# Kernel tuning notes

Measured on AMD Instinct MI355X. Metric: run time of the kernel, lower is better.

Reference implementation:

```python
import jax, jax.numpy as jnp
import numpy as np


def setup_inputs() -> dict:
    key = jax.random.key(0)
    k1, k2, k3, k4 = jax.random.split(key, 4)
    B, T_dec, T_enc, H2 = 8, 64, 512, 512  # H2 = 2*hiddenSize
    encoderOutput = jax.random.normal(k1, (B, T_enc, H2), dtype=jnp.float32)
    decoderInput = jax.random.normal(k2, (B, T_dec, H2), dtype=jnp.float32)
    # fc: Linear(4H -> 2H); torch weight layout [out, in] = [2H, 4H]
    W = jax.random.normal(k3, (H2, 2 * H2), dtype=jnp.float32) * (1.0 / np.sqrt(2 * H2))
    b = jax.random.normal(k4, (H2,), dtype=jnp.float32) * 0.01
    return {"encoderOutput": encoderOutput, "decoderInput": decoderInput, "W": W, "b": b}


def reference(encoderOutput, decoderInput, W, b):
    # Original: for each (i, j), fc(cat(dec[:,i], enc[:,j])) then log_softmax over
    # the FEATURE dim (dim=1 of the flattened [-1, 2H] tensor), then
    # context[:, i] = sum_j log_softmax(...) * enc[:, j].
    H2 = encoderOutput.shape[-1]
    W_dec = W[:, :H2]   # columns multiplying the decoder half of the concat
    W_enc = W[:, H2:]   # columns multiplying the encoder half
    dec_part = jnp.einsum('bid,od->bio', decoderInput, W_dec)   # [B, T_dec, 2H]
    enc_part = jnp.einsum('bjd,od->bjo', encoderOutput, W_enc)  # [B, T_enc, 2H]
    logits = dec_part[:, :, None, :] + enc_part[:, None, :, :] + b  # [B, T_dec, T_enc, 2H]
    alpha = jax.nn.log_softmax(logits, axis=-1)  # softmax over feature dim, as in source
    context = jnp.einsum('bijd,bjd->bid', alpha, encoderOutput)  # [B, T_dec, 2H]
    return context
```

## Files before the change

kernel.cpp:

```cpp
#include <hip/hip_runtime.h>


namespace {
constexpr int kH  = 512;
constexpr int kTD = 64;
constexpr int kTE = 512;
constexpr int kB  = 8;
constexpr int kRD = kB * kTD;
constexpr int kRE = kB * kTE;
}

typedef __attribute__((ext_vector_type(8))) short short8;
typedef __attribute__((ext_vector_type(4))) float floatx4;

__device__ __forceinline__ unsigned short f2bf(float x) {
    unsigned u = __float_as_uint(x);
    u += 0x7fffu + ((u >> 16) & 1u);
    return (unsigned short)(u >> 16);
}
__device__ __forceinline__ float bf2f(unsigned short h) {
    return __uint_as_float(((unsigned)h) << 16);
}

__global__ __launch_bounds__(256) void fused_cast(
    const float* __restrict__ W, const float* __restrict__ dec,
    const float* __restrict__ enc,
    unsigned short* __restrict__ Wd, unsigned short* __restrict__ We,
    unsigned short* __restrict__ dec_bf,
    unsigned short* __restrict__ enc_bf, unsigned short* __restrict__ encT,
    float* __restrict__ S1, float* __restrict__ S2)
{
    const int blk = blockIdx.x, t = threadIdx.x;
    if (blk < 2048) {
        const int idx = blk * 256 + t;
        const int row = idx >> 10, col = idx & 1023;
        const unsigned short v = f2bf(W[idx]);
        if (col < kH) Wd[row * kH + col] = v;
        else          We[row * kH + (col - kH)] = v;
        if (idx < kRD * kH) dec_bf[idx] = f2bf(dec[idx]);
        if (idx < kB * kH) { S1[idx] = 0.f; S2[idx] = 0.f; }
    } else {
        __shared__ unsigned short s[32][33];
        const int tid = blk - 2048;
        const int b = tid >> 8, rem = tid & 255;
        const int j0 = (rem >> 4) * 32, d0 = (rem & 15) * 32;
        const int tx = t & 31, ty = t >> 5;
        const float* src = enc + ((size_t)b * kTE + j0) * kH + d0;
        unsigned short* edst = enc_bf + ((size_t)b * kTE + j0) * kH + d0;
#pragma unroll
        for (int jj = 0; jj < 32; jj += 8) {
            const unsigned short h = f2bf(src[(size_t)(ty + jj) * kH + tx]);
            s[ty + jj][tx] = h;
            edst[(size_t)(ty + jj) * kH + tx] = h;
        }
        __syncthreads();
        unsigned short* tdst = encT + ((size_t)b * kH + d0) * kTE + j0;
#pragma unroll
        for (int dd = 0; dd < 32; dd += 8)
            tdst[(size_t)(ty + dd) * kTE + tx] = s[tx][ty + dd];
    }
}

__global__ __launch_bounds__(256) void gemm1(
    const unsigned short* __restrict__ enc_bf,
    const unsigned short* __restrict__ dec_bf,
    const unsigned short* __restrict__ Wd,
    const unsigned short* __restrict__ We,
    const float* __restrict__ bias,
    unsigned short* __restrict__ part_bf, unsigned short* __restrict__ uv)
{
    const int tile = blockIdx.x;
    const int ns = tile & 7, ms = tile >> 3;
    const int t = threadIdx.x, w = t >> 6, l = t & 63;
    const int qm = w >> 1, qn = w & 1;
    const int lr = l & 15, lq = l >> 4;
    const bool isenc = (ms >= 8);
    const unsigned short* A = isenc ? (enc_bf + (size_t)(ms - 8) * 64 * kH)
                                    : (dec_bf + (size_t)ms * 64 * kH);
    const unsigned short* Bw = isenc ? We : Wd;
    const unsigned short* a0 = A + (size_t)(qm * 32 + lr) * kH + lq * 8;
    const unsigned short* b0 = Bw + (size_t)(ns * 64 + qn * 32 + lr) * kH + lq * 8;

    floatx4 acc[2][2];
#pragma unroll
    for (int m = 0; m < 2; ++m)
#pragma unroll
        for (int n = 0; n < 2; ++n) acc[m][n] = (floatx4){0.f, 0.f, 0.f, 0.f};

    for (int k0 = 0; k0 < kH; k0 += 32) {
        short8 af[2], bf[2];
#pragma unroll
        for (int m = 0; m < 2; ++m) af[m] = *(const short8*)(a0 + (size_t)m * 16 * kH + k0);
#pragma unroll
        for (int n = 0; n < 2; ++n) bf[n] = *(const short8*)(b0 + (size_t)n * 16 * kH + k0);
#pragma unroll
        for (int m = 0; m < 2; ++m)
#pragma unroll
            for (int n = 0; n < 2; ++n)
                acc[m][n] = __builtin_amdgcn_mfma_f32_16x16x32_bf16(af[m], bf[n], acc[m][n], 0, 0, 0);
    }

    const int rowbase = ms * 64 + qm * 32, colbase = ns * 64 + qn * 32;
#pragma unroll
    for (int n = 0; n < 2; ++n) {
        const int col = colbase + n * 16 + lr;
        const float bv = isenc ? bias[col] : 0.f;
#pragma unroll
        for (int m = 0; m < 2; ++m) {
            const int row0 = rowbase + m * 16 + lq * 4;
#pragma unroll
            for (int r = 0; r < 4; ++r) {
                const float v = acc[m][n][r];
                const size_t off = (size_t)(row0 + r) * kH + col;
                part_bf[off] = f2bf(v);
                uv[off]      = f2bf(__expf(v + bv));
            }
        }
    }
}

__global__ __launch_bounds__(256) void lse_s1s2(
    const unsigned short* __restrict__ uv, unsigned short* __restrict__ lse_bf,
    const float* __restrict__ enc, const unsigned short* __restrict__ part_bf,
    float* __restrict__ S1, float* __restrict__ S2)
{
    __shared__ float red[4][16][68];
    const int blk = blockIdx.x, t = threadIdx.x;
    if (blk < 256) {
        const int b = blk >> 5, rem = blk & 31;
        const int it = rem >> 3, jt = rem & 7;
        const int w = t >> 6, l = t & 63;
        const int lr = l & 15, lq = l >> 4;
        const unsigned short* ua = uv + (size_t)(b * 64 + it * 16 + lr) * kH + w * 128 + lq * 8;
        const unsigned short* vb = uv + (size_t)(kRD + b * kTE + jt * 64 + lr) * kH + w * 128 + lq * 8;

        floatx4 acc[4];
#pragma unroll
        for (int n = 0; n < 4; ++n) acc[n] = (floatx4){0.f, 0.f, 0.f, 0.f};
#pragma unroll
        for (int k0 = 0; k0 < 128; k0 += 32) {
            const short8 af = *(const short8*)(ua + k0);
#pragma unroll
            for (int n = 0; n < 4; ++n)
                acc[n] = __builtin_amdgcn_mfma_f32_16x16x32_bf16(
                    af, *(const short8*)(vb + (size_t)n * 16 * kH + k0), acc[n], 0, 0, 0);
        }
#pragma unroll
        for (int n = 0; n < 4; ++n)
#pragma unroll
            for (int r = 0; r < 4; ++r)
                red[w][lq * 4 + r][n * 16 + lr] = acc[n][r];
        __syncthreads();
        const int i = t >> 4, j0 = (t & 15) * 4;
        float4 s = *(const float4*)&red[0][i][j0];
        const float4 s1 = *(const float4*)&red[1][i][j0];
        const float4 s2 = *(const float4*)&red[2][i][j0];
        const float4 s3 = *(const float4*)&red[3][i][j0];
        s.x += s1.x + s2.x + s3.x; s.y += s1.y + s2.y + s3.y;
        s.z += s1.z + s2.z + s3.z; s.w += s1.w + s2.w + s3.w;
        ushort4 o;
        o.x = f2bf(__logf(s.x)); o.y = f2bf(__logf(s.y));
        o.z = f2bf(__logf(s.z)); o.w = f2bf(__logf(s.w));
        *(ushort4*)(lse_bf + (size_t)(b * kTD + it * 16 + i) * kTE + jt * 64 + j0) = o;
    } else {
        const int blk2 = blk - 256;
        const int jc = blk2 & 15, b = (blk2 >> 4) & 7, dh = blk2 >> 7;
        const int d = dh * 256 + t;
        const float* e = enc + ((size_t)b * kTE + jc * 32) * kH + d;
        const unsigned short* p = part_bf + (size_t)(kRD + b * kTE + jc * 32) * kH + d;
        float s1 = 0.f, s2 = 0.f;
#pragma unroll 4
        for (int j = 0; j < 32; ++j) {
            const float ev = e[(size_t)j * kH];
            const float pv = bf2f(p[(size_t)j * kH]);
            s1 += ev;
            s2 = fmaf(pv, ev, s2);
        }
        atomicAdd(&S1[b * kH + d], s1);
        atomicAdd(&S2[b * kH + d], s2);
    }
}

__global__ __launch_bounds__(256) void final_k(
    const unsigned short* __restrict__ lse_bf,
    const unsigned short* __restrict__ encT,
    const unsigned short* __restrict__ part_bf,
    const float* __restrict__ bias,
    const float* __restrict__ S1, const float* __restrict__ S2,
    float* __restrict__ out)
{
    __shared__ float red[4][16][68];
    const int blk = blockIdx.x, t = threadIdx.x;
    const int b = blk >> 5, rem = blk & 31;
    const int it = rem >> 3, dt = rem & 7;
    const int w = t >> 6, l = t & 63;
    const int lr = l & 15, lq = l >> 4;
    const unsigned short* la = lse_bf + (size_t)(b * kTD + it * 16 + lr) * kTE + w * 128 + lq * 8;
    const unsigned short* eb = encT + ((size_t)b * kH + dt * 64 + lr) * kTE + w * 128 + lq * 8;

    floatx4 acc[4];
#pragma unroll
    for (int n = 0; n < 4; ++n) acc[n] = (floatx4){0.f, 0.f, 0.f, 0.f};
#pragma unroll
    for (int k0 = 0; k0 < 128; k0 += 32) {
        const short8 af = *(const short8*)(la + k0);
#pragma unroll
        for (int n = 0; n < 4; ++n)
            acc[n] = __builtin_amdgcn_mfma_f32_16x16x32_bf16(
                af, *(const short8*)(eb + (size_t)n * 16 * kTE + k0), acc[n], 0, 0, 0);
    }
#pragma unroll
    for (int n = 0; n < 4; ++n)
#pragma unroll
        for (int r = 0; r < 4; ++r)
            red[w][lq * 4 + r][n * 16 + lr] = acc[n][r];
    __syncthreads();
    const int i = t >> 4, d0 = (t & 15) * 4;
    float4 m = *(const float4*)&red[0][i][d0];
    const float4 m1 = *(const float4*)&red[1][i][d0];
    const float4 m2 = *(const float4*)&red[2][i][d0];
    const float4 m3 = *(const float4*)&red[3][i][d0];
    m.x += m1.x + m2.x + m3.x; m.y += m1.y + m2.y + m3.y;
    m.z += m1.z + m2.z + m3.z; m.w += m1.w + m2.w + m3.w;

    const int gd = dt * 64 + d0;
    const float4 s1 = *(const float4*)(S1 + b * kH + gd);
    const float4 s2 = *(const float4*)(S2 + b * kH + gd);
    const float4 bi = *(const float4*)(bias + gd);
    const int row = b * kTD + it * 16 + i;
    const ushort4 dp = *(const ushort4*)(part_bf + (size_t)row * kH + gd);
    float4 o;
    o.x = fmaf(bf2f(dp.x) + bi.x, s1.x, s2.x) - m.x;
    o.y = fmaf(bf2f(dp.y) + bi.y, s1.y, s2.y) - m.y;
    o.z = fmaf(bf2f(dp.z) + bi.z, s1.z, s2.z) - m.z;
    o.w = fmaf(bf2f(dp.w) + bi.w, s1.w, s2.w) - m.w;
    *(float4*)(out + (size_t)row * kH + gd) = o;
}

extern "C" void kernel_launch(void* const* d_in, const int* in_sizes, int n_in,
                              void* d_out, int out_size, void* d_ws, size_t ws_size,
                              hipStream_t stream)
{
    (void)in_sizes; (void)n_in; (void)out_size; (void)ws_size;
    const float* enc  = (const float*)d_in[0];
    const float* dec  = (const float*)d_in[1];
    const float* W    = (const float*)d_in[2];
    const float* bias = (const float*)d_in[3];
    float* out = (float*)d_out;

    char* base = (char*)d_ws;
    unsigned short* part_bf = (unsigned short*)(base);
    unsigned short* uv      = (unsigned short*)(base + 4718592);
    unsigned short* enc_bf  = (unsigned short*)(base + 9437184);
    unsigned short* encT    = (unsigned short*)(base + 13631488);
    unsigned short* dec_bf  = (unsigned short*)(base + 17825792);
    unsigned short* Wd      = (unsigned short*)(base + 18350080);
    unsigned short* We      = (unsigned short*)(base + 18874368);
    unsigned short* lse_bf  = (unsigned short*)(base + 19398656);
    float*          S1      = (float*)(base + 19922944);
    float*          S2      = (float*)(base + 19939328);

    fused_cast<<<4096, 256, 0, stream>>>(W, dec, enc, Wd, We, dec_bf,
                                         enc_bf, encT, S1, S2);
    gemm1<<<576, 256, 0, stream>>>(enc_bf, dec_bf, Wd, We, bias, part_bf, uv);
    lse_s1s2<<<512, 256, 0, stream>>>(uv, lse_bf, enc, part_bf, S1, S2);
    final_k<<<256, 256, 0, stream>>>(lse_bf, encT, part_bf, bias, S1, S2, out);
}
```

Before: 102.7 us.

## Store bf16 operands in MFMA fragment-tiled layout across all kernels

Every bf16 intermediate (W halves, decoder, encoder, transposed encoder, exp-logits, lse) is now written in a fragment-packed layout, so each lane loads one contiguous 16-byte fragment and each wave reads one contiguous 1 KB block instead of strided rows. The cast kernel is rewritten to do vectorized float4 loads with packed short8 stores, which cuts its grid from 4096 to 1408 blocks. The gemm1 epilogue is staged through shared memory so its stores are vectorized. This adds an LDS round trip and more complex indexing, and the layouts of the producer and consumer kernels must agree exactly.

```diff
diff --git a/kernel.cpp b/kernel.cpp
--- a/kernel.cpp
+++ b/kernel.cpp
@@ -21,108 +21,161 @@
 __device__ __forceinline__ float bf2f(unsigned short h) {
     return __uint_as_float(((unsigned)h) << 16);
 }
+__device__ __forceinline__ size_t fragTile(int rtile, int kt) {
+    return ((size_t)rtile * 16 + kt) * 512;
+}
+__device__ __forceinline__ short8 pack8(float4 a, float4 b) {
+    short8 r;
+    r[0] = (short)f2bf(a.x); r[1] = (short)f2bf(a.y);
+    r[2] = (short)f2bf(a.z); r[3] = (short)f2bf(a.w);
+    r[4] = (short)f2bf(b.x); r[5] = (short)f2bf(b.y);
+    r[6] = (short)f2bf(b.z); r[7] = (short)f2bf(b.w);
+    return r;
+}
 
 __global__ __launch_bounds__(256) void fused_cast(
     const float* __restrict__ W, const float* __restrict__ dec,
     const float* __restrict__ enc,
-    unsigned short* __restrict__ Wd, unsigned short* __restrict__ We,
-    unsigned short* __restrict__ dec_bf,
-    unsigned short* __restrict__ enc_bf, unsigned short* __restrict__ encT,
-    float* __restrict__ S1, float* __restrict__ S2)
+    unsigned short* __restrict__ Wd_f, unsigned short* __restrict__ We_f,
+    unsigned short* __restrict__ dec_f,
+    unsigned short* __restrict__ enc_f, unsigned short* __restrict__ encT_f,
+    float* __restrict__ S12)
 {
     const int blk = blockIdx.x, t = threadIdx.x;
-    if (blk < 2048) {
-        const int idx = blk * 256 + t;
-        const int row = idx >> 10, col = idx & 1023;
-        const unsigned short v = f2bf(W[idx]);
-        if (col < kH) Wd[row * kH + col] = v;
-        else          We[row * kH + (col - kH)] = v;
-        if (idx < kRD * kH) dec_bf[idx] = f2bf(dec[idx]);
-        if (idx < kB * kH) { S1[idx] = 0.f; S2[idx] = 0.f; }
+    const int w = t >> 6, l = t & 63;
+    const int lr = l & 15, lc = l >> 4;
+    if (blk < 256) {
+        const int gw = blk * 4 + w;
+        const int sel = gw >> 9, rem = gw & 511;
+        const int ot = rem >> 4, kt = rem & 15;
+        const int o = ot * 16 + lr;
+        const float* src = W + (size_t)o * 1024 + sel * 512 + kt * 32 + lc * 8;
+        const float4 v0 = *(const float4*)src;
+        const float4 v1 = *(const float4*)(src + 4);
+        unsigned short* dst = (sel ? We_f : Wd_f) + fragTile(ot, kt) + l * 8;
+        *(short8*)dst = pack8(v0, v1);
+        if (blk < 32) S12[blk * 256 + t] = 0.f;
+    } else if (blk < 384) {
+        const int gw = (blk - 256) * 4 + w;
+        const int rt = gw >> 4, kt = gw & 15;
+        const int r = rt * 16 + lr;
+        const float* src = dec + (size_t)r * kH + kt * 32 + lc * 8;
+        const float4 v0 = *(const float4*)src;
+        const float4 v1 = *(const float4*)(src + 4);
+        *(short8*)(dec_f + fragTile(rt, kt) + l * 8) = pack8(v0, v1);
     } else {
-        __shared__ unsigned short s[32][33];
-        const int tid = blk - 2048;
-        const int b = tid >> 8, rem = tid & 255;
-        const int j0 = (rem >> 4) * 32, d0 = (rem & 15) * 32;
-        const int tx = t & 31, ty = t >> 5;
-        const float* src = enc + ((size_t)b * kTE + j0) * kH + d0;
-        unsigned short* edst = enc_bf + ((size_t)b * kTE + j0) * kH + d0;
-#pragma unroll
-        for (int jj = 0; jj < 32; jj += 8) {
-            const unsigned short h = f2bf(src[(size_t)(ty + jj) * kH + tx]);
-            s[ty + jj][tx] = h;
-            edst[(size_t)(ty + jj) * kH + tx] = h;
-        }
+        __shared__ unsigned short s[64][36];
+        const int e = blk - 384;
+        const int kt = e & 15, jt = (e >> 4) & 7, b = e >> 7;
+        const int j0 = jt * 64, d0 = kt * 32;
+        const int jl = w * 16 + lr;
+        const float* src = enc + ((size_t)(b * kTE + j0 + jl)) * kH + d0 + lc * 8;
+        const float4 v0 = *(const float4*)src;
+        const float4 v1 = *(const float4*)(src + 4);
+        const short8 p = pack8(v0, v1);
+        *(short8*)(enc_f + fragTile(b * 32 + jt * 4 + w, kt) + l * 8) = p;
+#pragma unroll
+        for (int i = 0; i < 8; ++i) s[jl][lc * 8 + i] = (unsigned short)p[i];
         __syncthreads();
-        unsigned short* tdst = encT + ((size_t)b * kH + d0) * kTE + j0;
-#pragma unroll
-        for (int dd = 0; dd < 32; dd += 8)
-            tdst[(size_t)(ty + dd) * kTE + tx] = s[tx][ty + dd];
+        const int dt = w >> 1, jc = w & 1;
+        const int dl = dt * 16 + lr;
+        const int j8 = jc * 32 + lc * 8;
+        short8 v;
+#pragma unroll
+        for (int i = 0; i < 8; ++i) v[i] = (short)s[j8 + i][dl];
+        *(short8*)(encT_f + fragTile(b * 32 + kt * 2 + dt, jt * 2 + jc) + l * 8) = v;
     }
 }
 
 __global__ __launch_bounds__(256) void gemm1(
-    const unsigned short* __restrict__ enc_bf,
-    const unsigned short* __restrict__ dec_bf,
-    const unsigned short* __restrict__ Wd,
-    const unsigned short* __restrict__ We,
+    const unsigned short* __restrict__ enc_f,
+    const unsigned short* __restrict__ dec_f,
+    const unsigned short* __restrict__ Wd_f,
+    const unsigned short* __restrict__ We_f,
     const float* __restrict__ bias,
-    unsigned short* __restrict__ part_bf, unsigned short* __restrict__ uv)
-{
+    unsigned short* __restrict__ part_bf, unsigned short* __restrict__ uv_f)
+{
+    __shared__ float As[64][68];
     const int tile = blockIdx.x;
     const int ns = tile & 7, ms = tile >> 3;
     const int t = threadIdx.x, w = t >> 6, l = t & 63;
     const int qm = w >> 1, qn = w & 1;
+    const bool isenc = (ms >= 8);
+    const unsigned short* A = isenc ? enc_f : dec_f;
+    const unsigned short* Bw = isenc ? We_f : Wd_f;
+    const int art = (isenc ? (ms - 8) : ms) * 4 + qm * 2;
+    const int brt = ns * 4 + qn * 2;
+
+    floatx4 acc[2][2];
+#pragma unroll
+    for (int m = 0; m < 2; ++m)
+#pragma unroll
+        for (int n = 0; n < 2; ++n) acc[m][n] = (floatx4){0.f, 0.f, 0.f, 0.f};
+
+    for (int kt = 0; kt < 16; ++kt) {
+        short8 af[2], bfr[2];
+#pragma unroll
+        for (int m = 0; m < 2; ++m)
+            af[m] = *(const short8*)(A + fragTile(art + m, kt) + l * 8);
+#pragma unroll
+        for (int n = 0; n < 2; ++n)
+            bfr[n] = *(const short8*)(Bw + fragTile(brt + n, kt) + l * 8);
+#pragma unroll
+        for (int m = 0; m < 2; ++m)
+#pragma unroll
+            for (int n = 0; n < 2; ++n)
+                acc[m][n] = __builtin_amdgcn_mfma_f32_16x16x32_bf16(af[m], bfr[n], acc[m][n], 0, 0, 0);
+    }
+
     const int lr = l & 15, lq = l >> 4;
-    const bool isenc = (ms >= 8);
-    const unsigned short* A = isenc ? (enc_bf + (size_t)(ms - 8) * 64 * kH)
-                                    : (dec_bf + (size_t)ms * 64 * kH);
-    const unsigned short* Bw = isenc ? We : Wd;
-    const unsigned short* a0 = A + (size_t)(qm * 32 + lr) * kH + lq * 8;
-    const unsigned short* b0 = Bw + (size_t)(ns * 64 + qn * 32 + lr) * kH + lq * 8;
-
-    floatx4 acc[2][2];
 #pragma unroll
     for (int m = 0; m < 2; ++m)
 #pragma unroll
-        for (int n = 0; n < 2; ++n) acc[m][n] = (floatx4){0.f, 0.f, 0.f, 0.f};
-
-    for (int k0 = 0; k0 < kH; k0 += 32) {
-        short8 af[2], bf[2];
-#pragma unroll
-        for (int m = 0; m < 2; ++m) af[m] = *(const short8*)(a0 + (size_t)m * 16 * kH + k0);
-#pragma unroll
-        for (int n = 0; n < 2; ++n) bf[n] = *(const short8*)(b0 + (size_t)n * 16 * kH + k0);
-#pragma unroll
-        for (int m = 0; m < 2; ++m)
-#pragma unroll
-            for (int n = 0; n < 2; ++n)
-                acc[m][n] = __builtin_amdgcn_mfma_f32_16x16x32_bf16(af[m], bf[n], acc[m][n], 0, 0, 0);
-    }
-
-    const int rowbase = ms * 64 + qm * 32, colbase = ns * 64 + qn * 32;
-#pragma unroll
-    for (int n = 0; n < 2; ++n) {
-        const int col = colbase + n * 16 + lr;
-        const float bv = isenc ? bias[col] : 0.f;
-#pragma unroll
-        for (int m = 0; m < 2; ++m) {
-            const int row0 = rowbase + m * 16 + lq * 4;
-#pragma unroll
-            for (int r = 0; r < 4; ++r) {
-                const float v = acc[m][n][r];
-                const size_t off = (size_t)(row0 + r) * kH + col;
-                part_bf[off] = f2bf(v);
-                uv[off]      = f2bf(__expf(v + bv));
-            }
+        for (int n = 0; n < 2; ++n)
+#pragma unroll
+            for (int r = 0; r < 4; ++r)
+                As[qm * 32 + m * 16 + lq * 4 + r][qn * 32 + n * 16 + lr] = acc[m][n][r];
+    __syncthreads();
+
+    const int rowbase = ms * 64, colbase = ns * 64;
+#pragma unroll
+    for (int h = 0; h < 2; ++h) {
+        const int a = h * 256 + t;
+        const int row = a >> 3, cc = (a & 7) * 8;
+        const float4 v0 = *(const float4*)&As[row][cc];
+        const float4 v1 = *(const float4*)&As[row][cc + 4];
+        *(short8*)(part_bf + (size_t)(rowbase + row) * kH + colbase + cc) = pack8(v0, v1);
+    }
+#pragma unroll
+    for (int h = 0; h < 2; ++h) {
+        const int s = h * 256 + t;
+        const int rt = s >> 7, kc = (s >> 6) & 1, fl = s & 63;
+        const int row = rt * 16 + (fl & 15);
+        const int col = kc * 32 + (fl >> 4) * 8;
+        const float4 v0 = *(const float4*)&As[row][col];
+        const float4 v1 = *(const float4*)&As[row][col + 4];
+        float4 b0 = make_float4(0.f, 0.f, 0.f, 0.f), b1 = b0;
+        if (isenc) {
+            b0 = *(const float4*)(bias + colbase + col);
+            b1 = *(const float4*)(bias + colbase + col + 4);
         }
+        short8 u;
+        u[0] = (short)f2bf(__expf(v0.x + b0.x));
+        u[1] = (short)f2bf(__expf(v0.y + b0.y));
+        u[2] = (short)f2bf(__expf(v0.z + b0.z));
+        u[3] = (short)f2bf(__expf(v0.w + b0.w));
+        u[4] = (short)f2bf(__expf(v1.x + b1.x));
+        u[5] = (short)f2bf(__expf(v1.y + b1.y));
+        u[6] = (short)f2bf(__expf(v1.z + b1.z));
+        u[7] = (short)f2bf(__expf(v1.w + b1.w));
+        *(short8*)(uv_f + fragTile(ms * 4 + rt, ns * 2 + kc) + fl * 8) = u;
     }
 }
 
 __global__ __launch_bounds__(256) void lse_s1s2(
-    const unsigned short* __restrict__ uv, unsigned short* __restrict__ lse_bf,
+    const unsigned short* __restrict__ uv_f, unsigned short* __restrict__ lse_f,
     const float* __restrict__ enc, const unsigned short* __restrict__ part_bf,
-    float* __restrict__ S1, float* __restrict__ S2)
+    float* __restrict__ S12)
 {
     __shared__ float red[4][16][68];
     const int blk = blockIdx.x, t = threadIdx.x;
@@ -130,38 +183,42 @@
         const int b = blk >> 5, rem = blk & 31;
         const int it = rem >> 3, jt = rem & 7;
         const int w = t >> 6, l = t & 63;
-        const int lr = l & 15, lq = l >> 4;
-        const unsigned short* ua = uv + (size_t)(b * 64 + it * 16 + lr) * kH + w * 128 + lq * 8;
-        const unsigned short* vb = uv + (size_t)(kRD + b * kTE + jt * 64 + lr) * kH + w * 128 + lq * 8;
+        const int art = b * 4 + it;
+        const int vrt0 = 32 + b * 32 + jt * 4;
 
         floatx4 acc[4];
 #pragma unroll
         for (int n = 0; n < 4; ++n) acc[n] = (floatx4){0.f, 0.f, 0.f, 0.f};
 #pragma unroll
-        for (int k0 = 0; k0 < 128; k0 += 32) {
-            const short8 af = *(const short8*)(ua + k0);
+        for (int kk = 0; kk < 4; ++kk) {
+            const int kt = w * 4 + kk;
+            const short8 af = *(const short8*)(uv_f + fragTile(art, kt) + l * 8);
 #pragma unroll
             for (int n = 0; n < 4; ++n)
                 acc[n] = __builtin_amdgcn_mfma_f32_16x16x32_bf16(
-                    af, *(const short8*)(vb + (size_t)n * 16 * kH + k0), acc[n], 0, 0, 0);
+                    af, *(const short8*)(uv_f + fragTile(vrt0 + n, kt) + l * 8), acc[n], 0, 0, 0);
         }
+        const int lr = l & 15, lq = l >> 4;
 #pragma unroll
         for (int n = 0; n < 4; ++n)
 #pragma unroll
             for (int r = 0; r < 4; ++r)
                 red[w][lq * 4 + r][n * 16 + lr] = acc[n][r];
         __syncthreads();
-        const int i = t >> 4, j0 = (t & 15) * 4;
-        float4 s = *(const float4*)&red[0][i][j0];
-        const float4 s1 = *(const float4*)&red[1][i][j0];
-        const float4 s2 = *(const float4*)&red[2][i][j0];
-        const float4 s3 = *(const float4*)&red[3][i][j0];
-        s.x += s1.x + s2.x + s3.x; s.y += s1.y + s2.y + s3.y;
-        s.z += s1.z + s2.z + s3.z; s.w += s1.w + s2.w + s3.w;
+        const int s = t >> 1, h = t & 1;
+        const int kc = s >> 6, fl = s & 63;
+        const int i = fl & 15;
+        const int j = kc * 32 + (fl >> 4) * 8 + h * 4;
+        float4 sum = *(const float4*)&red[0][i][j];
+        const float4 s1 = *(const float4*)&red[1][i][j];
+        const float4 s2 = *(const float4*)&red[2][i][j];
+        const float4 s3 = *(const float4*)&red[3][i][j];
+        sum.x += s1.x + s2.x + s3.x; sum.y += s1.y + s2.y + s3.y;
+        sum.z += s1.z + s2.z + s3.z; sum.w += s1.w + s2.w + s3.w;
         ushort4 o;
-        o.x = f2bf(__logf(s.x)); o.y = f2bf(__logf(s.y));
-        o.z = f2bf(__logf(s.z)); o.w = f2bf(__logf(s.w));
-        *(ushort4*)(lse_bf + (size_t)(b * kTD + it * 16 + i) * kTE + jt * 64 + j0) = o;
+        o.x = f2bf(__logf(sum.x)); o.y = f2bf(__logf(sum.y));
+        o.z = f2bf(__logf(sum.z)); o.w = f2bf(__logf(sum.w));
+        *(ushort4*)(lse_f + fragTile(b * 4 + it, jt * 2 + kc) + fl * 8 + h * 4) = o;
     } else {
         const int blk2 = blk - 256;
         const int jc = blk2 & 15, b = (blk2 >> 4) & 7, dh = blk2 >> 7;
@@ -176,17 +233,17 @@
             s1 += ev;
             s2 = fmaf(pv, ev, s2);
         }
-        atomicAdd(&S1[b * kH + d], s1);
-        atomicAdd(&S2[b * kH + d], s2);
+        atomicAdd(&S12[b * kH + d], s1);
+        atomicAdd(&S12[4096 + b * kH + d], s2);
     }
 }
 
 __global__ __launch_bounds__(256) void final_k(
-    const unsigned short* __restrict__ lse_bf,
-    const unsigned short* __restrict__ encT,
+    const unsigned short* __restrict__ lse_f,
+    const unsigned short* __restrict__ encT_f,
     const unsigned short* __restrict__ part_bf,
     const float* __restrict__ bias,
-    const float* __restrict__ S1, const float* __restrict__ S2,
+    const float* __restrict__ S12,
     float* __restrict__ out)
 {
     __shared__ float red[4][16][68];
@@ -194,21 +251,22 @@
     const int b = blk >> 5, rem = blk & 31;
     const int it = rem >> 3, dt = rem & 7;
     const int w = t >> 6, l = t & 63;
-    const int lr = l & 15, lq = l >> 4;
-    const unsigned short* la = lse_bf + (size_t)(b * kTD + it * 16 + lr) * kTE + w * 128 + lq * 8;
-    const unsigned short* eb = encT + ((size_t)b * kH + dt * 64 + lr) * kTE + w * 128 + lq * 8;
+    const int art = b * 4 + it;
+    const int brt0 = b * 32 + dt * 4;
 
     floatx4 acc[4];
 #pragma unroll
     for (int n = 0; n < 4; ++n) acc[n] = (floatx4){0.f, 0.f, 0.f, 0.f};
 #pragma unroll
-    for (int k0 = 0; k0 < 128; k0 += 32) {
-        const short8 af = *(const short8*)(la + k0);
+    for (int kk = 0; kk < 4; ++kk) {
+        const int kt = w * 4 + kk;
+        const short8 af = *(const short8*)(lse_f + fragTile(art, kt) + l * 8);
 #pragma unroll
         for (int n = 0; n < 4; ++n)
             acc[n] = __builtin_amdgcn_mfma_f32_16x16x32_bf16(
-                af, *(const short8*)(eb + (size_t)n * 16 * kTE + k0), acc[n], 0, 0, 0);
-    }
+                af, *(const short8*)(encT_f + fragTile(brt0 + n, kt) + l * 8), acc[n], 0, 0, 0);
+    }
+    const int lr = l & 15, lq = l >> 4;
 #pragma unroll
     for (int n = 0; n < 4; ++n)
 #pragma unroll
@@ -224,8 +282,8 @@
     m.z += m1.z + m2.z + m3.z; m.w += m1.w + m2.w + m3.w;
 
     const int gd = dt * 64 + d0;
-    const float4 s1 = *(const float4*)(S1 + b * kH + gd);
-    const float4 s2 = *(const float4*)(S2 + b * kH + gd);
+    const float4 s1 = *(const float4*)(S12 + b * kH + gd);
+    const float4 s2 = *(const float4*)(S12 + 4096 + b * kH + gd);
     const float4 bi = *(const float4*)(bias + gd);
     const int row = b * kTD + it * 16 + i;
     const ushort4 dp = *(const ushort4*)(part_bf + (size_t)row * kH + gd);
@@ -250,19 +308,18 @@
 
     char* base = (char*)d_ws;
     unsigned short* part_bf = (unsigned short*)(base);
-    unsigned short* uv      = (unsigned short*)(base + 4718592);
-    unsigned short* enc_bf  = (unsigned short*)(base + 9437184);
-    unsigned short* encT    = (unsigned short*)(base + 13631488);
-    unsigned short* dec_bf  = (unsigned short*)(base + 17825792);
-    unsigned short* Wd      = (unsigned short*)(base + 18350080);
-    unsigned short* We      = (unsigned short*)(base + 18874368);
-    unsigned short* lse_bf  = (unsigned short*)(base + 19398656);
-    float*          S1      = (float*)(base + 19922944);
-    float*          S2      = (float*)(base + 19939328);
-
-    fused_cast<<<4096, 256, 0, stream>>>(W, dec, enc, Wd, We, dec_bf,
-                                         enc_bf, encT, S1, S2);
-    gemm1<<<576, 256, 0, stream>>>(enc_bf, dec_bf, Wd, We, bias, part_bf, uv);
-    lse_s1s2<<<512, 256, 0, stream>>>(uv, lse_bf, enc, part_bf, S1, S2);
-    final_k<<<256, 256, 0, stream>>>(lse_bf, encT, part_bf, bias, S1, S2, out);
-}
+    unsigned short* uv_f    = (unsigned short*)(base + 4718592);
+    unsigned short* enc_f   = (unsigned short*)(base + 9437184);
+    unsigned short* encT_f  = (unsigned short*)(base + 13631488);
+    unsigned short* dec_f   = (unsigned short*)(base + 17825792);
+    unsigned short* Wd_f    = (unsigned short*)(base + 18350080);
+    unsigned short* We_f    = (unsigned short*)(base + 18874368);
+    unsigned short* lse_f   = (unsigned short*)(base + 19398656);
+    float*          S12     = (float*)(base + 19922944);
+
+    fused_cast<<<1408, 256, 0, stream>>>(W, dec, enc, Wd_f, We_f, dec_f,
+                                         enc_f, encT_f, S12);
+    gemm1<<<576, 256, 0, stream>>>(enc_f, dec_f, Wd_f, We_f, bias, part_bf, uv_f);
+    lse_s1s2<<<512, 256, 0, stream>>>(uv_f, lse_f, enc, part_bf, S12);
+    final_k<<<256, 256, 0, stream>>>(lse_f, encT_f, part_bf, bias, S12, out);
+}
```

New measurement: 91.26 us. -11.1%, faster.
